# Kernel tuning notes

Hardware: AMD Instinct MI355X
Metric: run time of the kernel (lower is better)

Reference implementation:

```python
import jax, jax.numpy as jnp
import numpy as np

B, N, C, M = 8, 65536, 64, 64


def _build_frequency_lattice(num_modes: int) -> np.ndarray:
    candidates = []
    radius = 1
    while len(candidates) < num_modes * 2:
        for kx in range(-radius, radius + 1):
            for ky in range(-radius, radius + 1):
                if kx == 0 and ky == 0:
                    continue
                candidates.append((abs(kx) + abs(ky), kx, ky))
        radius += 1
    candidates.sort(key=lambda it: (it[0], abs(it[1]), abs(it[2]), it[1], it[2]))
    unique, seen = [], set()
    for _, kx, ky in candidates:
        if (kx, ky) in seen:
            continue
        seen.add((kx, ky))
        unique.append((kx, ky))
        if len(unique) >= num_modes:
            break
    return np.asarray(unique, dtype=np.float32)  # [M, 2]


def setup_inputs() -> dict:
    key = jax.random.key(0)
    k1, k2, k3, k4 = jax.random.split(key, 4)
    inputs = jax.random.normal(k1, (B, N, C), dtype=jnp.float32)
    coords = jax.random.uniform(k2, (B, N, 2), dtype=jnp.float32)
    scale = 1.0 / C
    # complex weight (M, C) split into real/imag float parts
    weight_re = scale * jax.random.normal(k3, (M, C), dtype=jnp.float32)
    weight_im = scale * jax.random.normal(k4, (M, C), dtype=jnp.float32)
    frequencies = jnp.asarray(_build_frequency_lattice(M))  # [M, 2]
    return {"inputs": inputs, "coords": coords, "weight_re": weight_re,
            "weight_im": weight_im, "frequencies": frequencies}


def reference(inputs, coords, weight_re, weight_im, frequencies):
    # phase: [B, N, M]
    phase = 2.0 * jnp.pi * jnp.einsum('bnc,mc->bnm', coords, frequencies)
    basis = jnp.exp(1j * phase.astype(jnp.complex64))  # [B, N, M]
    # project onto modes: [B, M, C], normalized by N
    coeffs = jnp.einsum('bnm,bnc->bmc', jnp.conj(basis), inputs.astype(jnp.complex64))
    coeffs = coeffs / N
    weight = weight_re + 1j * weight_im  # [M, C]
    mixed = coeffs * weight[None, :, :]  # [B, M, C]
    reconstructed = jnp.einsum('bnm,bmd->bnd', basis, mixed)  # [B, N, C]
    return jnp.real(reconstructed)
```

## Files before the change

kernel.cpp:

```cpp
#include <hip/hip_runtime.h>
#include <hip/hip_bf16.h>

#define BB 8
#define NN 65536
#define CC 64
#define MM 64

#define TWO_PI 6.283185307179586476925286766559f

typedef __attribute__((ext_vector_type(8))) short bf16x8;
typedef __attribute__((ext_vector_type(4))) float f32x4;
typedef unsigned int u32;
typedef unsigned short u16;

__device__ inline u32 pk_bf2(float a, float b) {
  __hip_bfloat162 h = __float22bfloat162_rn(make_float2(a, b));
  u32 r;
  __builtin_memcpy(&r, &h, 4);
  return r;
}

__device__ inline u16 sbf(float a) {
  __hip_bfloat16 h = __float2bfloat16(a);
  u16 r;
  __builtin_memcpy(&r, &h, 2);
  return r;
}

__global__ __launch_bounds__(256) void proj_mfma(
    const float* __restrict__ inputs,
    const float* __restrict__ coords,
    const float* __restrict__ freqs,
    float* __restrict__ accg)
{
  __shared__ __align__(16) u16 As[128 * 64];
  __shared__ __align__(16) u16 Xs[64 * 64];

  const int tid  = threadIdx.x;
  const int b    = blockIdx.x >> 7;
  const int nbase = (blockIdx.x & 127) * 512;
  const int lane = tid & 63;
  const int wave = tid >> 6;
  const int l15  = lane & 15;
  const int quad = lane >> 4;

  const int bm = tid & 63;
  const int pg = tid >> 6;
  const float fx = freqs[2 * bm];
  const float fy = freqs[2 * bm + 1];

  const int np = tid & 15;
  const int cq = tid >> 4;

  const float4* c4 = (const float4*)coords;
  const float4* x4 = (const float4*)inputs;

  f32x4 acc[2][4];
#pragma unroll
  for (int rt = 0; rt < 2; ++rt)
#pragma unroll
    for (int ct = 0; ct < 4; ++ct) acc[rt][ct] = (f32x4){0.f, 0.f, 0.f, 0.f};

  for (int s = 0; s < 8; ++s) {
    const int n0 = nbase + s * 64;

#pragma unroll
    for (int g = 0; g < 2; ++g) {
      const int k8 = pg * 2 + g;
      const int nb = n0 + k8 * 8;
      u32 cpk[4], spk[4];
#pragma unroll
      for (int jj = 0; jj < 4; ++jj) {
        const float4 cc = c4[(size_t)(b * NN + nb + jj * 2) >> 1];
        const float ph0 = TWO_PI * fmaf(cc.x, fx, cc.y * fy);
        const float ph1 = TWO_PI * fmaf(cc.z, fx, cc.w * fy);
        float s0, c0, s1, c1;
        __sincosf(ph0, &s0, &c0);
        __sincosf(ph1, &s1, &c1);
        cpk[jj] = pk_bf2(c0, c1);
        spk[jj] = pk_bf2(s0, s1);
      }
      *(uint4*)&As[bm * 64 + ((k8 + bm) & 7) * 8] =
          make_uint4(cpk[0], cpk[1], cpk[2], cpk[3]);
      const int rs = bm + 64;
      *(uint4*)&As[rs * 64 + ((k8 + rs) & 7) * 8] =
          make_uint4(spk[0], spk[1], spk[2], spk[3]);
    }

#pragma unroll
    for (int half = 0; half < 2; ++half) {
      const int k = half * 32 + 2 * np;
      const int n = n0 + k;
      const float4 x0 = x4[(size_t)(b * NN + n) * 16 + cq];
      const float4 x1 = x4[(size_t)(b * NN + n + 1) * 16 + cq];
      const int k8 = k >> 3, koff = k & 7;
      const float* p0 = (const float*)&x0;
      const float* p1 = (const float*)&x1;
#pragma unroll
      for (int j = 0; j < 4; ++j) {
        const int c = cq * 4 + j;
        *(u32*)&Xs[c * 64 + ((k8 + c) & 7) * 8 + koff] = pk_bf2(p0[j], p1[j]);
      }
    }
    __syncthreads();

#pragma unroll
    for (int kk = 0; kk < 2; ++kk) {
      const int k8q = kk * 4 + quad;
      const int r0 = wave * 32 + l15;
      const int r1 = r0 + 16;
      const bf16x8 a0 = *(const bf16x8*)&As[r0 * 64 + ((k8q + r0) & 7) * 8];
      const bf16x8 a1 = *(const bf16x8*)&As[r1 * 64 + ((k8q + r1) & 7) * 8];
      bf16x8 bfr[4];
#pragma unroll
      for (int ct = 0; ct < 4; ++ct) {
        const int c = ct * 16 + l15;
        bfr[ct] = *(const bf16x8*)&Xs[c * 64 + ((k8q + c) & 7) * 8];
      }
#pragma unroll
      for (int ct = 0; ct < 4; ++ct) {
        acc[0][ct] = __builtin_amdgcn_mfma_f32_16x16x32_bf16(a0, bfr[ct], acc[0][ct], 0, 0, 0);
        acc[1][ct] = __builtin_amdgcn_mfma_f32_16x16x32_bf16(a1, bfr[ct], acc[1][ct], 0, 0, 0);
      }
    }
    __syncthreads();
  }

  float* ab = accg + (size_t)b * 128 * 64;
#pragma unroll
  for (int rt = 0; rt < 2; ++rt)
#pragma unroll
    for (int ct = 0; ct < 4; ++ct)
#pragma unroll
      for (int r = 0; r < 4; ++r) {
        const int mrow = wave * 32 + rt * 16 + quad * 4 + r;
        const int c = ct * 16 + l15;
        atomicAdd(&ab[mrow * 64 + c], acc[rt][ct][r]);
      }
}

__global__ __launch_bounds__(256) void mix_kernel(
    const float* __restrict__ accg, const float* __restrict__ wre,
    const float* __restrict__ wim, u16* __restrict__ w2t)
{
  const int b = blockIdx.x;
  const float invN = 1.0f / (float)NN;
  const float* ab = accg + (size_t)b * 128 * 64;
  u16* wb_ = w2t + (size_t)b * 64 * 128;
  for (int idx = threadIdx.x; idx < MM * CC; idx += 256) {
    const int m = idx >> 6, c = idx & 63;
    const float gre = ab[m * 64 + c];
    const float gim = ab[(64 + m) * 64 + c];
    const float wr = wre[m * 64 + c], wi = wim[m * 64 + c];
    wb_[c * 128 + m]      = sbf((gre * wr + gim * wi) * invN);
    wb_[c * 128 + 64 + m] = sbf((gim * wr - gre * wi) * invN);
  }
}

__global__ __launch_bounds__(256) void recon_mfma(
    const float* __restrict__ coords,
    const u16* __restrict__ w2t,
    const float* __restrict__ freqs,
    float* __restrict__ out)
{
  __shared__ __align__(16) u16 Ps[128 * 128];
  __shared__ float sfx[64], sfy[64];

  const int tid  = threadIdx.x;
  const int b    = blockIdx.x >> 7;
  const int tg   = blockIdx.x & 127;
  const int lane = tid & 63;
  const int wave = tid >> 6;
  const int l15  = lane & 15;
  const int quad = lane >> 4;

  if (tid < 64) { sfx[tid] = freqs[2 * tid]; sfy[tid] = freqs[2 * tid + 1]; }

  bf16x8 wb[4][4];
#pragma unroll
  for (int kc = 0; kc < 4; ++kc)
#pragma unroll
    for (int ct = 0; ct < 4; ++ct)
      wb[kc][ct] = *(const bf16x8*)&w2t[((size_t)b * 64 + ct * 16 + l15) * 128 +
                                        kc * 32 + quad * 8];
  __syncthreads();

  const int p  = tid & 127;
  const int mg = (tid >> 7) * 32;
  const float2* c2 = (const float2*)coords;

  for (int t = 0; t < 4; ++t) {
    const int n0 = (tg * 4 + t) * 128;

    const float2 cc = c2[(size_t)b * NN + n0 + p];
#pragma unroll
    for (int g = 0; g < 4; ++g) {
      u32 cpk[4], spk[4];
#pragma unroll
      for (int jj = 0; jj < 4; ++jj) {
        const int m = mg + g * 8 + jj * 2;
        const float ph0 = TWO_PI * fmaf(cc.x, sfx[m], cc.y * sfy[m]);
        const float ph1 = TWO_PI * fmaf(cc.x, sfx[m + 1], cc.y * sfy[m + 1]);
        float s0, c0, s1, c1;
        __sincosf(ph0, &s0, &c0);
        __sincosf(ph1, &s1, &c1);
        cpk[jj] = pk_bf2(c0, c1);
        spk[jj] = pk_bf2(s0, s1);
      }
      const int k8c = (mg >> 3) + g;
      const int k8s = k8c + 8;
      *(uint4*)&Ps[p * 128 + ((k8c + p) & 15) * 8] =
          make_uint4(cpk[0], cpk[1], cpk[2], cpk[3]);
      *(uint4*)&Ps[p * 128 + ((k8s + p) & 15) * 8] =
          make_uint4(spk[0], spk[1], spk[2], spk[3]);
    }
    __syncthreads();

    f32x4 acc[2][4];
#pragma unroll
    for (int rt = 0; rt < 2; ++rt)
#pragma unroll
      for (int ct = 0; ct < 4; ++ct) acc[rt][ct] = (f32x4){0.f, 0.f, 0.f, 0.f};

#pragma unroll
    for (int kc = 0; kc < 4; ++kc) {
      const int k8q = kc * 4 + quad;
      const int r0 = wave * 32 + l15;
      const int r1 = r0 + 16;
      const bf16x8 a0 = *(const bf16x8*)&Ps[r0 * 128 + ((k8q + r0) & 15) * 8];
      const bf16x8 a1 = *(const bf16x8*)&Ps[r1 * 128 + ((k8q + r1) & 15) * 8];
#pragma unroll
      for (int ct = 0; ct < 4; ++ct) {
        acc[0][ct] = __builtin_amdgcn_mfma_f32_16x16x32_bf16(a0, wb[kc][ct], acc[0][ct], 0, 0, 0);
        acc[1][ct] = __builtin_amdgcn_mfma_f32_16x16x32_bf16(a1, wb[kc][ct], acc[1][ct], 0, 0, 0);
      }
    }

    float* ob = out + ((size_t)b * NN + n0) * 64;
#pragma unroll
    for (int rt = 0; rt < 2; ++rt)
#pragma unroll
      for (int ct = 0; ct < 4; ++ct)
#pragma unroll
        for (int r = 0; r < 4; ++r) {
          const int row = wave * 32 + rt * 16 + quad * 4 + r;
          ob[row * 64 + ct * 16 + l15] = acc[rt][ct][r];
        }
    __syncthreads();
  }
}

extern "C" void kernel_launch(void* const* d_in, const int* in_sizes, int n_in,
                              void* d_out, int out_size, void* d_ws, size_t ws_size,
                              hipStream_t stream) {
  const float* inputs = (const float*)d_in[0];
  const float* coords = (const float*)d_in[1];
  const float* wre    = (const float*)d_in[2];
  const float* wim    = (const float*)d_in[3];
  const float* freqs  = (const float*)d_in[4];
  float* out = (float*)d_out;

  float* accg = (float*)d_ws;
  u16*   w2t  = (u16*)((char*)d_ws + (size_t)BB * 128 * 64 * 4);

  hipMemsetAsync(accg, 0, (size_t)BB * 128 * 64 * sizeof(float), stream);
  proj_mfma<<<dim3(BB * 128), dim3(256), 0, stream>>>(inputs, coords, freqs, accg);
  mix_kernel<<<dim3(BB), dim3(256), 0, stream>>>(accg, wre, wim, w2t);
  recon_mfma<<<dim3(BB * 128), dim3(256), 0, stream>>>(coords, w2t, freqs, out);
}
```

Measured before the change: 286.3 us.

## Double-buffer LDS tiles and replace global atomics with partial-sum reduction

Both MFMA kernels now double-buffer their LDS tiles: global loads for the next step are issued before the current MFMAs, and the sincos/bf16 staging for the next tile happens after them, removing one barrier per step. The projection kernel writes per-block partial sums instead of atomically adding into a zeroed buffer. The mix kernel now reduces those 64 partials per batch across 128 blocks, so the memset is dropped. Grids are halved with twice the work per block, and LDS use doubles, which may reduce occupancy and leave fewer blocks to fill the device.

Measured after the change: 266.3 us. 7.0% less time.

```diff
diff --git a/kernel.cpp b/kernel.cpp
--- a/kernel.cpp
+++ b/kernel.cpp
@@ -27,22 +27,25 @@
   return r;
 }
 
+#define CH1 64
+#define STEPS1 16
+
 __global__ __launch_bounds__(256) void proj_mfma(
     const float* __restrict__ inputs,
     const float* __restrict__ coords,
     const float* __restrict__ freqs,
-    float* __restrict__ accg)
+    float* __restrict__ partial)
 {
-  __shared__ __align__(16) u16 As[128 * 64];
-  __shared__ __align__(16) u16 Xs[64 * 64];
-
-  const int tid  = threadIdx.x;
-  const int b    = blockIdx.x >> 7;
-  const int nbase = (blockIdx.x & 127) * 512;
-  const int lane = tid & 63;
-  const int wave = tid >> 6;
-  const int l15  = lane & 15;
-  const int quad = lane >> 4;
+  __shared__ __align__(16) u16 As[2][128 * 64];
+  __shared__ __align__(16) u16 Xs[2][64 * 64];
+
+  const int tid   = threadIdx.x;
+  const int b     = blockIdx.x >> 6;
+  const int nbase = (blockIdx.x & 63) * 1024;
+  const int lane  = tid & 63;
+  const int wave  = tid >> 6;
+  const int l15   = lane & 15;
+  const int quad  = lane >> 4;
 
   const int bm = tid & 63;
   const int pg = tid >> 6;
@@ -55,23 +58,33 @@
   const float4* c4 = (const float4*)coords;
   const float4* x4 = (const float4*)inputs;
 
-  f32x4 acc[2][4];
-#pragma unroll
-  for (int rt = 0; rt < 2; ++rt)
-#pragma unroll
-    for (int ct = 0; ct < 4; ++ct) acc[rt][ct] = (f32x4){0.f, 0.f, 0.f, 0.f};
-
-  for (int s = 0; s < 8; ++s) {
-    const int n0 = nbase + s * 64;
-
+  float4 cpre[2][4];
+  float4 xpre[2][2];
+
+  auto load_step = [&](int s) {
+#pragma unroll
+    for (int g = 0; g < 2; ++g) {
+      const int nb = nbase + s * 64 + (pg * 2 + g) * 8;
+#pragma unroll
+      for (int jj = 0; jj < 4; ++jj)
+        cpre[g][jj] = c4[(size_t)(b * NN + nb + jj * 2) >> 1];
+    }
+#pragma unroll
+    for (int half = 0; half < 2; ++half) {
+      const int n = nbase + s * 64 + half * 32 + 2 * np;
+      xpre[half][0] = x4[(size_t)(b * NN + n) * 16 + cq];
+      xpre[half][1] = x4[(size_t)(b * NN + n + 1) * 16 + cq];
+    }
+  };
+
+  auto stage_step = [&](int buf) {
 #pragma unroll
     for (int g = 0; g < 2; ++g) {
       const int k8 = pg * 2 + g;
-      const int nb = n0 + k8 * 8;
       u32 cpk[4], spk[4];
 #pragma unroll
       for (int jj = 0; jj < 4; ++jj) {
-        const float4 cc = c4[(size_t)(b * NN + nb + jj * 2) >> 1];
+        const float4 cc = cpre[g][jj];
         const float ph0 = TWO_PI * fmaf(cc.x, fx, cc.y * fy);
         const float ph1 = TWO_PI * fmaf(cc.z, fx, cc.w * fy);
         float s0, c0, s1, c1;
@@ -80,42 +93,52 @@
         cpk[jj] = pk_bf2(c0, c1);
         spk[jj] = pk_bf2(s0, s1);
       }
-      *(uint4*)&As[bm * 64 + ((k8 + bm) & 7) * 8] =
+      *(uint4*)&As[buf][bm * 64 + ((k8 + bm) & 7) * 8] =
           make_uint4(cpk[0], cpk[1], cpk[2], cpk[3]);
       const int rs = bm + 64;
-      *(uint4*)&As[rs * 64 + ((k8 + rs) & 7) * 8] =
+      *(uint4*)&As[buf][rs * 64 + ((k8 + rs) & 7) * 8] =
           make_uint4(spk[0], spk[1], spk[2], spk[3]);
     }
-
 #pragma unroll
     for (int half = 0; half < 2; ++half) {
       const int k = half * 32 + 2 * np;
-      const int n = n0 + k;
-      const float4 x0 = x4[(size_t)(b * NN + n) * 16 + cq];
-      const float4 x1 = x4[(size_t)(b * NN + n + 1) * 16 + cq];
       const int k8 = k >> 3, koff = k & 7;
-      const float* p0 = (const float*)&x0;
-      const float* p1 = (const float*)&x1;
+      const float* p0 = (const float*)&xpre[half][0];
+      const float* p1 = (const float*)&xpre[half][1];
 #pragma unroll
       for (int j = 0; j < 4; ++j) {
         const int c = cq * 4 + j;
-        *(u32*)&Xs[c * 64 + ((k8 + c) & 7) * 8 + koff] = pk_bf2(p0[j], p1[j]);
-      }
-    }
-    __syncthreads();
+        *(u32*)&Xs[buf][c * 64 + ((k8 + c) & 7) * 8 + koff] = pk_bf2(p0[j], p1[j]);
+      }
+    }
+  };
+
+  f32x4 acc[2][4];
+#pragma unroll
+  for (int rt = 0; rt < 2; ++rt)
+#pragma unroll
+    for (int ct = 0; ct < 4; ++ct) acc[rt][ct] = (f32x4){0.f, 0.f, 0.f, 0.f};
+
+  load_step(0);
+  stage_step(0);
+  __syncthreads();
+
+  for (int s = 0; s < STEPS1; ++s) {
+    const int cur = s & 1;
+    if (s + 1 < STEPS1) load_step(s + 1);
 
 #pragma unroll
     for (int kk = 0; kk < 2; ++kk) {
       const int k8q = kk * 4 + quad;
       const int r0 = wave * 32 + l15;
       const int r1 = r0 + 16;
-      const bf16x8 a0 = *(const bf16x8*)&As[r0 * 64 + ((k8q + r0) & 7) * 8];
-      const bf16x8 a1 = *(const bf16x8*)&As[r1 * 64 + ((k8q + r1) & 7) * 8];
+      const bf16x8 a0 = *(const bf16x8*)&As[cur][r0 * 64 + ((k8q + r0) & 7) * 8];
+      const bf16x8 a1 = *(const bf16x8*)&As[cur][r1 * 64 + ((k8q + r1) & 7) * 8];
       bf16x8 bfr[4];
 #pragma unroll
       for (int ct = 0; ct < 4; ++ct) {
         const int c = ct * 16 + l15;
-        bfr[ct] = *(const bf16x8*)&Xs[c * 64 + ((k8q + c) & 7) * 8];
+        bfr[ct] = *(const bf16x8*)&Xs[cur][c * 64 + ((k8q + c) & 7) * 8];
       }
 #pragma unroll
       for (int ct = 0; ct < 4; ++ct) {
@@ -123,10 +146,12 @@
         acc[1][ct] = __builtin_amdgcn_mfma_f32_16x16x32_bf16(a1, bfr[ct], acc[1][ct], 0, 0, 0);
       }
     }
+
+    if (s + 1 < STEPS1) stage_step(1 - cur);
     __syncthreads();
   }
 
-  float* ab = accg + (size_t)b * 128 * 64;
+  float* pb = partial + (size_t)blockIdx.x * (128 * 64);
 #pragma unroll
   for (int rt = 0; rt < 2; ++rt)
 #pragma unroll
@@ -135,27 +160,33 @@
       for (int r = 0; r < 4; ++r) {
         const int mrow = wave * 32 + rt * 16 + quad * 4 + r;
         const int c = ct * 16 + l15;
-        atomicAdd(&ab[mrow * 64 + c], acc[rt][ct][r]);
+        pb[mrow * 64 + c] = acc[rt][ct][r];
       }
 }
 
 __global__ __launch_bounds__(256) void mix_kernel(
-    const float* __restrict__ accg, const float* __restrict__ wre,
-    const float* __restrict__ wim, u16* __restrict__ w2t)
+    const float* __restrict__ partial,
+    const float* __restrict__ wre, const float* __restrict__ wim,
+    u16* __restrict__ w2t)
 {
-  const int b = blockIdx.x;
+  const int idx = blockIdx.x * 256 + threadIdx.x;
+  const int b = idx >> 12;
+  const int m = (idx >> 6) & 63;
+  const int c = idx & 63;
+  const float* pb = partial + (size_t)b * CH1 * 8192;
+  float gre = 0.f, gim = 0.f;
+  for (int k = 0; k < CH1; ++k) {
+    gre += pb[(size_t)k * 8192 + m * 64 + c];
+    gim += pb[(size_t)k * 8192 + (64 + m) * 64 + c];
+  }
   const float invN = 1.0f / (float)NN;
-  const float* ab = accg + (size_t)b * 128 * 64;
+  const float wr = wre[m * 64 + c], wi = wim[m * 64 + c];
   u16* wb_ = w2t + (size_t)b * 64 * 128;
-  for (int idx = threadIdx.x; idx < MM * CC; idx += 256) {
-    const int m = idx >> 6, c = idx & 63;
-    const float gre = ab[m * 64 + c];
-    const float gim = ab[(64 + m) * 64 + c];
-    const float wr = wre[m * 64 + c], wi = wim[m * 64 + c];
-    wb_[c * 128 + m]      = sbf((gre * wr + gim * wi) * invN);
-    wb_[c * 128 + 64 + m] = sbf((gim * wr - gre * wi) * invN);
-  }
-}
+  wb_[c * 128 + m]      = sbf((gre * wr + gim * wi) * invN);
+  wb_[c * 128 + 64 + m] = sbf((gim * wr - gre * wi) * invN);
+}
+
+#define TILES2 8
 
 __global__ __launch_bounds__(256) void recon_mfma(
     const float* __restrict__ coords,
@@ -163,16 +194,16 @@
     const float* __restrict__ freqs,
     float* __restrict__ out)
 {
-  __shared__ __align__(16) u16 Ps[128 * 128];
+  __shared__ __align__(16) u16 Ps[2][128 * 128];
   __shared__ float sfx[64], sfy[64];
 
-  const int tid  = threadIdx.x;
-  const int b    = blockIdx.x >> 7;
-  const int tg   = blockIdx.x & 127;
-  const int lane = tid & 63;
-  const int wave = tid >> 6;
-  const int l15  = lane & 15;
-  const int quad = lane >> 4;
+  const int tid   = threadIdx.x;
+  const int b     = blockIdx.x >> 6;
+  const int nbase = (blockIdx.x & 63) * 1024;
+  const int lane  = tid & 63;
+  const int wave  = tid >> 6;
+  const int l15   = lane & 15;
+  const int quad  = lane >> 4;
 
   if (tid < 64) { sfx[tid] = freqs[2 * tid]; sfy[tid] = freqs[2 * tid + 1]; }
 
@@ -189,10 +220,7 @@
   const int mg = (tid >> 7) * 32;
   const float2* c2 = (const float2*)coords;
 
-  for (int t = 0; t < 4; ++t) {
-    const int n0 = (tg * 4 + t) * 128;
-
-    const float2 cc = c2[(size_t)b * NN + n0 + p];
+  auto stage_tile = [&](int buf, float2 cc) {
 #pragma unroll
     for (int g = 0; g < 4; ++g) {
       u32 cpk[4], spk[4];
@@ -209,12 +237,23 @@
       }
       const int k8c = (mg >> 3) + g;
       const int k8s = k8c + 8;
-      *(uint4*)&Ps[p * 128 + ((k8c + p) & 15) * 8] =
+      *(uint4*)&Ps[buf][p * 128 + ((k8c + p) & 15) * 8] =
           make_uint4(cpk[0], cpk[1], cpk[2], cpk[3]);
-      *(uint4*)&Ps[p * 128 + ((k8s + p) & 15) * 8] =
+      *(uint4*)&Ps[buf][p * 128 + ((k8s + p) & 15) * 8] =
           make_uint4(spk[0], spk[1], spk[2], spk[3]);
     }
-    __syncthreads();
+  };
+
+  float2 cpre = c2[(size_t)b * NN + nbase + p];
+  stage_tile(0, cpre);
+  __syncthreads();
+
+  for (int t = 0; t < TILES2; ++t) {
+    const int cur = t & 1;
+    const int n0 = nbase + t * 128;
+
+    float2 cnext;
+    if (t + 1 < TILES2) cnext = c2[(size_t)b * NN + n0 + 128 + p];
 
     f32x4 acc[2][4];
 #pragma unroll
@@ -227,14 +266,16 @@
       const int k8q = kc * 4 + quad;
       const int r0 = wave * 32 + l15;
       const int r1 = r0 + 16;
-      const bf16x8 a0 = *(const bf16x8*)&Ps[r0 * 128 + ((k8q + r0) & 15) * 8];
-      const bf16x8 a1 = *(const bf16x8*)&Ps[r1 * 128 + ((k8q + r1) & 15) * 8];
+      const bf16x8 a0 = *(const bf16x8*)&Ps[cur][r0 * 128 + ((k8q + r0) & 15) * 8];
+      const bf16x8 a1 = *(const bf16x8*)&Ps[cur][r1 * 128 + ((k8q + r1) & 15) * 8];
 #pragma unroll
       for (int ct = 0; ct < 4; ++ct) {
         acc[0][ct] = __builtin_amdgcn_mfma_f32_16x16x32_bf16(a0, wb[kc][ct], acc[0][ct], 0, 0, 0);
         acc[1][ct] = __builtin_amdgcn_mfma_f32_16x16x32_bf16(a1, wb[kc][ct], acc[1][ct], 0, 0, 0);
       }
     }
+
+    if (t + 1 < TILES2) stage_tile(1 - cur, cnext);
 
     float* ob = out + ((size_t)b * NN + n0) * 64;
 #pragma unroll
@@ -246,6 +287,7 @@
           const int row = wave * 32 + rt * 16 + quad * 4 + r;
           ob[row * 64 + ct * 16 + l15] = acc[rt][ct][r];
         }
+
     __syncthreads();
   }
 }
@@ -260,11 +302,10 @@
   const float* freqs  = (const float*)d_in[4];
   float* out = (float*)d_out;
 
-  float* accg = (float*)d_ws;
-  u16*   w2t  = (u16*)((char*)d_ws + (size_t)BB * 128 * 64 * 4);
-
-  hipMemsetAsync(accg, 0, (size_t)BB * 128 * 64 * sizeof(float), stream);
-  proj_mfma<<<dim3(BB * 128), dim3(256), 0, stream>>>(inputs, coords, freqs, accg);
-  mix_kernel<<<dim3(BB), dim3(256), 0, stream>>>(accg, wre, wim, w2t);
-  recon_mfma<<<dim3(BB * 128), dim3(256), 0, stream>>>(coords, w2t, freqs, out);
-}
+  float* partial = (float*)d_ws;
+  u16*   w2t     = (u16*)((char*)d_ws + (size_t)BB * CH1 * 128 * 64 * 4);
+
+  proj_mfma<<<dim3(BB * CH1), dim3(256), 0, stream>>>(inputs, coords, freqs, partial);
+  mix_kernel<<<dim3(128), dim3(256), 0, stream>>>(partial, wre, wim, w2t);
+  recon_mfma<<<dim3(BB * CH1), dim3(256), 0, stream>>>(coords, w2t, freqs, out);
+}
```
